# Optimization experiments

Hardware: AMD Instinct MI355X
Metric: run time of the kernel (lower is better)

The kernel has to match this reference:

```python
import jax, jax.numpy as jnp
import numpy as np

DIM = 192
HEADS = 6
WS = (4, 4, 4)
N = 64          # prod(WS)
NW = 64         # windows per sample
BATCH = 2048    # num_windows * B
CPB_HIDDEN = 512


def _make_rpb_tables():
    space = len(WS)
    coords = [np.arange(-(w - 1), w, dtype=np.float32) for w in WS]
    rpb = np.stack(np.meshgrid(*coords, indexing='ij'))  # (3, 7,7,7)
    for i in range(space):
        rpb[i] = rpb[i] / (WS[i] - 1)
    rpb = np.moveaxis(rpb, 0, -1)[None]  # (1,7,7,7,3)
    rpb = 8.0 * rpb
    rpb = np.sign(rpb) * np.log2(np.abs(rpb) + 1.0) / np.log2(8.0)
    grid = np.stack(np.meshgrid(*[np.arange(w) for w in WS], indexing='ij')).reshape(space, -1)  # (3, N)
    dists = grid[:, :, None] - grid[:, None, :]  # (3, N, N)
    for i in range(space):
        center = max(int(np.prod([2 * w - 1 for w in WS[i + 1:]])), 1)
        dists[i] = (dists[i] + WS[i] - 1) * center
    rpb_idx = dists.sum(0)  # (N, N), values in [0, 343)
    return jnp.asarray(rpb, jnp.float32), jnp.asarray(rpb_idx, jnp.int32)


def setup_inputs() -> dict:
    key = jax.random.key(0)
    ks = jax.random.split(key, 8)
    rpb, rpb_idx = _make_rpb_tables()
    s = 0.02
    return {
        'x': jax.random.normal(ks[0], (BATCH, N, DIM), jnp.float32),
        'mask': jnp.zeros((NW, N, N), jnp.float32),
        'rpb': rpb,
        'rpb_idx': rpb_idx,
        'cpb_w1': jax.random.normal(ks[1], (CPB_HIDDEN, len(WS)), jnp.float32) * s,
        'cpb_b1': jnp.zeros((CPB_HIDDEN,), jnp.float32),
        'cpb_w2': jax.random.normal(ks[2], (HEADS, CPB_HIDDEN), jnp.float32) * s,
        'qkv_w': jax.random.normal(ks[3], (3 * DIM, DIM), jnp.float32) * s,
        'qkv_b': jnp.zeros((3 * DIM,), jnp.float32),
        'proj_w': jax.random.normal(ks[4], (DIM, DIM), jnp.float32) * s,
        'proj_b': jnp.zeros((DIM,), jnp.float32),
        'logit_scale': jnp.log(10.0 * jnp.ones((HEADS, 1, 1), jnp.float32)),
    }


def reference(x, mask, rpb, rpb_idx, cpb_w1, cpb_b1, cpb_w2, qkv_w, qkv_b,
              proj_w, proj_b, logit_scale):
    B, n, C = x.shape
    H = logit_scale.shape[0]
    hd = C // H
    # qkv projection -> (3, B, H, n, hd)
    qkv = (x @ qkv_w.T + qkv_b).reshape(B, n, 3, H, hd).transpose(2, 0, 3, 1, 4)
    q, k, v = qkv[0], qkv[1], qkv[2]
    # continuous position bias MLP: (1,7,7,7,3) -> (1,7,7,7,H) -> gather -> (1,H,n,n)
    h1 = jax.nn.relu(rpb @ cpb_w1.T + cpb_b1)
    bias = (h1 @ cpb_w2.T).reshape(-1, H)            # (343, H)
    bias = bias[rpb_idx.reshape(-1)].reshape(n, n, H)
    bias = 16.0 * jax.nn.sigmoid(bias)
    bias = bias.transpose(2, 0, 1)[None]             # (1, H, n, n)
    # cosine attention
    qn = q / jnp.maximum(jnp.linalg.norm(q, axis=-1, keepdims=True), 1e-12)
    kn = k / jnp.maximum(jnp.linalg.norm(k, axis=-1, keepdims=True), 1e-12)
    scale = jnp.exp(jnp.minimum(logit_scale, jnp.log(jnp.float32(100.0))))  # clamp max=log(1/0.01)
    attn = jnp.einsum('bhnd,bhmd->bhnm', qn, kn) * scale + bias
    nW = mask.shape[0]
    attn = attn + jnp.tile(mask[:, None, :, :], (B // nW, 1, 1, 1))  # (B,1,n,n) broadcast over heads
    attn = jax.nn.softmax(attn, axis=-1)
    out = jnp.einsum('bhnm,bhmd->bhnd', attn, v)
    out = out.transpose(0, 2, 1, 3).reshape(B, n, C)  # heads-major concat (b n (h c))
    return out @ proj_w.T + proj_b
```

## Files before the change

### kernel.cpp

```cpp
#include <hip/hip_runtime.h>
#include <hip/hip_bf16.h>

#define DIM 192
#define HEADS 6
#define HD 32
#define NTOK 64
#define BATCH 2048
#define CPBH 512
#define TBL 343
#define NW 64

typedef unsigned int u32;
typedef __attribute__((ext_vector_type(8))) short b16x8;
typedef __attribute__((ext_vector_type(4))) float f32x4;

__device__ __forceinline__ unsigned short f2bf(float f) {
  union { __hip_bfloat16 h; unsigned short s; } cv;
  cv.h = __float2bfloat16(f);
  return cv.s;
}
__device__ __forceinline__ u32 pack2(float a, float b) {
  return (u32)f2bf(a) | ((u32)f2bf(b) << 16);
}
union FragU { u32 u[4]; b16x8 s; uint4 q; };

__device__ __forceinline__ b16x8 ld_frag_g(const u32* p) {
  FragU f; f.q = *(const uint4*)p; return f.s;
}

__global__ __launch_bounds__(64) void k_cpb1(
    const float* __restrict__ rpb, const float* __restrict__ w1,
    const float* __restrict__ b1, const float* __restrict__ w2,
    float* __restrict__ tab) {
  int t = blockIdx.x, lane = threadIdx.x;
  float r0 = rpb[t*3], r1 = rpb[t*3+1], r2 = rpb[t*3+2];
  float a[HEADS];
  #pragma unroll
  for (int h = 0; h < HEADS; ++h) a[h] = 0.f;
  #pragma unroll
  for (int kk = 0; kk < 8; ++kk) {
    int k = lane * 8 + kk;
    float hv = fmaf(r0, w1[k*3], fmaf(r1, w1[k*3+1], fmaf(r2, w1[k*3+2], b1[k])));
    hv = fmaxf(hv, 0.f);
    #pragma unroll
    for (int h = 0; h < HEADS; ++h) a[h] = fmaf(hv, w2[h*CPBH + k], a[h]);
  }
  #pragma unroll
  for (int h = 0; h < HEADS; ++h) {
    a[h] += __shfl_xor(a[h], 1);  a[h] += __shfl_xor(a[h], 2);
    a[h] += __shfl_xor(a[h], 4);  a[h] += __shfl_xor(a[h], 8);
    a[h] += __shfl_xor(a[h], 16); a[h] += __shfl_xor(a[h], 32);
  }
  if (lane == 0) {
    #pragma unroll
    for (int h = 0; h < HEADS; ++h) tab[t*HEADS + h] = a[h];
  }
}

__global__ void k_bm(const float* __restrict__ tab, const int* __restrict__ ridx,
                     const float* __restrict__ mask, float* __restrict__ bm) {
  int idx = blockIdx.x * blockDim.x + threadIdx.x;
  if (idx >= NW * HEADS * 4096) return;
  int ij = idx & 4095;
  int h = (idx >> 12) % HEADS;
  int nw = idx / (HEADS * 4096);
  float v = tab[ridx[ij] * HEADS + h];
  bm[idx] = 16.f / (1.f + __expf(-v)) + mask[nw * 4096 + ij];
}

__global__ void k_wcvt(const float* __restrict__ qkvw, const float* __restrict__ pw,
                       u32* __restrict__ wq, u32* __restrict__ wp) {
  int i = blockIdx.x * blockDim.x + threadIdx.x;
  if (i < 55296) {
    wq[i] = pack2(qkvw[2*i], qkvw[2*i+1]);
  } else if (i < 55296 + 18432) {
    int j = i - 55296;
    wp[j] = pack2(pw[2*j], pw[2*j+1]);
  }
}

__global__ __launch_bounds__(384) void k_qkv(
    const float* __restrict__ x, const u32* __restrict__ wq,
    const float* __restrict__ bias,
    u32* __restrict__ qo, u32* __restrict__ ko, u32* __restrict__ vT) {
  __shared__ u32 xl[NTOK * 101];
  const int tid = threadIdx.x;
  const int b = blockIdx.x;
  const float4* xg = (const float4*)(x + (size_t)b * (NTOK * DIM));
  for (int i = tid; i < (NTOK * DIM) / 4; i += 384) {
    float4 v = xg[i];
    int flat = i * 4, tok = flat / DIM, k = flat % DIM;
    xl[tok*101 + k/2]     = pack2(v.x, v.y);
    xl[tok*101 + k/2 + 1] = pack2(v.z, v.w);
  }
  __syncthreads();
  const int lane = tid & 63;
  const int wv = tid >> 6;
  const int m = lane & 15;
  const int qd = lane >> 4;
  const int sel = wv >> 1;
  u32* dst = (sel == 0) ? qo : (sel == 1) ? ko : vT;
  #pragma unroll 1
  for (int p = 0; p < 3; ++p) {
    const int h = (wv & 1) * 3 + p;
    const int jbase = wv * 96 + p * 32;
    b16x8 afr[2][6];
    float bv[2][4];
    #pragma unroll
    for (int half = 0; half < 2; ++half) {
      const u32* wp = wq + (size_t)(jbase + half*16 + m) * 96;
      #pragma unroll
      for (int ks = 0; ks < 6; ++ks) afr[half][ks] = ld_frag_g(wp + ks*16 + qd*4);
      #pragma unroll
      for (int r = 0; r < 4; ++r) bv[half][r] = bias[jbase + half*16 + qd*4 + r];
    }
    const size_t bh1024 = ((size_t)b * HEADS + h) * 1024;
    #pragma unroll 1
    for (int tp = 0; tp < 2; ++tp) {
      f32x4 acc[2][2];
      #pragma unroll
      for (int tt = 0; tt < 2; ++tt) {
        acc[tt][0] = (f32x4){0.f,0.f,0.f,0.f};
        acc[tt][1] = (f32x4){0.f,0.f,0.f,0.f};
      }
      #pragma unroll
      for (int ks = 0; ks < 6; ++ks) {
        #pragma unroll
        for (int tt = 0; tt < 2; ++tt) {
          b16x8 bfr = *(const b16x8*)(&xl[((tp*2+tt)*16 + m)*101 + ks*16 + qd*4]);
          acc[tt][0] = __builtin_amdgcn_mfma_f32_16x16x32_bf16(afr[0][ks], bfr, acc[tt][0], 0,0,0);
          acc[tt][1] = __builtin_amdgcn_mfma_f32_16x16x32_bf16(afr[1][ks], bfr, acc[tt][1], 0,0,0);
        }
      }
      #pragma unroll
      for (int tt = 0; tt < 2; ++tt) {
        const int t = tp*2 + tt;
        f32x4 acc0 = acc[tt][0], acc1 = acc[tt][1];
        #pragma unroll
        for (int r = 0; r < 4; ++r) { acc0[r] += bv[0][r]; acc1[r] += bv[1][r]; }
        if (sel < 2) {
          float ss = 0.f;
          #pragma unroll
          for (int r = 0; r < 4; ++r) ss = fmaf(acc0[r],acc0[r], fmaf(acc1[r],acc1[r], ss));
          ss += __shfl_xor(ss, 16);
          ss += __shfl_xor(ss, 32);
          float inv = 1.f / fmaxf(sqrtf(ss), 1e-12f);
          #pragma unroll
          for (int r = 0; r < 4; ++r) { acc0[r] *= inv; acc1[r] *= inv; }
          int tok = t*16 + m;
          u32* o = dst + bh1024 + tok*16;
          *(uint2*)(o + qd*2)     = make_uint2(pack2(acc0[0],acc0[1]), pack2(acc0[2],acc0[3]));
          *(uint2*)(o + 8 + qd*2) = make_uint2(pack2(acc1[0],acc1[1]), pack2(acc1[2],acc1[3]));
        } else {
          float p0[8];
          #pragma unroll
          for (int r = 0; r < 4; ++r) { p0[r] = acc0[r]; p0[4+r] = acc1[r]; }
          float pr[8];
          #pragma unroll
          for (int e = 0; e < 8; ++e) pr[e] = __shfl_xor(p0[e], 1);
          if ((m & 1) == 0) {
            #pragma unroll
            for (int e = 0; e < 8; ++e) {
              int d = (e >> 2)*16 + qd*4 + (e & 3);
              dst[bh1024 + d*32 + (t*16 + m)/2] = pack2(p0[e], pr[e]);
            }
          }
        }
      }
    }
  }
}

__global__ __launch_bounds__(384) void k_attn_proj(
    const u32* __restrict__ qo, const u32* __restrict__ ko, const u32* __restrict__ vT,
    const float* __restrict__ bm, const float* __restrict__ ls,
    const u32* __restrict__ wp, const float* __restrict__ pb,
    float* __restrict__ out) {
  __shared__ u32 pbuf[HEADS][64 * 35];
  __shared__ u32 aol[64 * 99];
  const int tid = threadIdx.x;
  const int b = blockIdx.x;
  const int h = tid >> 6;
  const int lane = tid & 63;
  const int m = lane & 15, qd = lane >> 4;
  const size_t bh1024 = ((size_t)b * HEADS + h) * 1024;

  b16x8 qfr[4], kfr[4];
  #pragma unroll
  for (int mt = 0; mt < 4; ++mt) qfr[mt] = ld_frag_g(qo + bh1024 + (mt*16 + m)*16 + qd*4);
  #pragma unroll
  for (int ct = 0; ct < 4; ++ct) kfr[ct] = ld_frag_g(ko + bh1024 + (ct*16 + m)*16 + qd*4);

  f32x4 s[4][4];
  #pragma unroll
  for (int mt = 0; mt < 4; ++mt)
    #pragma unroll
    for (int ct = 0; ct < 4; ++ct) {
      f32x4 z = {0.f,0.f,0.f,0.f};
      s[mt][ct] = __builtin_amdgcn_mfma_f32_16x16x32_bf16(qfr[mt], kfr[ct], z, 0,0,0);
    }

  const float sc = __expf(fminf(ls[h], 4.60517019f));
  const float* bmp = bm + ((size_t)(b & 63) * HEADS + h) * 4096;
  #pragma unroll
  for (int mt = 0; mt < 4; ++mt)
    #pragma unroll
    for (int ct = 0; ct < 4; ++ct) {
      #pragma unroll
      for (int r = 0; r < 4; ++r) {
        int row = mt*16 + qd*4 + r, col = ct*16 + m;
        s[mt][ct][r] = fmaf(s[mt][ct][r], sc, bmp[row*64 + col]);
      }
    }
  float rinv[4][4];
  u32* pbw = pbuf[h];
  #pragma unroll
  for (int mt = 0; mt < 4; ++mt) {
    #pragma unroll
    for (int r = 0; r < 4; ++r) {
      float mm = s[mt][0][r];
      #pragma unroll
      for (int ct = 1; ct < 4; ++ct) mm = fmaxf(mm, s[mt][ct][r]);
      mm = fmaxf(mm, __shfl_xor(mm, 1)); mm = fmaxf(mm, __shfl_xor(mm, 2));
      mm = fmaxf(mm, __shfl_xor(mm, 4)); mm = fmaxf(mm, __shfl_xor(mm, 8));
      float l = 0.f;
      #pragma unroll
      for (int ct = 0; ct < 4; ++ct) { s[mt][ct][r] = __expf(s[mt][ct][r] - mm); l += s[mt][ct][r]; }
      l += __shfl_xor(l, 1); l += __shfl_xor(l, 2);
      l += __shfl_xor(l, 4); l += __shfl_xor(l, 8);
      rinv[mt][r] = 1.f / l;
      int row = mt*16 + qd*4 + r;
      #pragma unroll
      for (int ct = 0; ct < 4; ++ct) {
        float pv = s[mt][ct][r];
        float pn = __shfl_xor(pv, 1);
        if ((m & 1) == 0) pbw[row*35 + ct*8 + (m >> 1)] = pack2(pv, pn);
      }
    }
  }
  b16x8 vfr[2][2];
  #pragma unroll
  for (int nt = 0; nt < 2; ++nt)
    #pragma unroll
    for (int ks = 0; ks < 2; ++ks)
      vfr[nt][ks] = ld_frag_g(vT + bh1024 + (nt*16 + m)*32 + ks*16 + qd*4);
  #pragma unroll
  for (int mt = 0; mt < 4; ++mt) {
    b16x8 pa0 = *(const b16x8*)(&pbw[(mt*16 + m)*35 + qd*4]);
    b16x8 pa1 = *(const b16x8*)(&pbw[(mt*16 + m)*35 + 16 + qd*4]);
    #pragma unroll
    for (int nt = 0; nt < 2; ++nt) {
      f32x4 o = {0.f,0.f,0.f,0.f};
      o = __builtin_amdgcn_mfma_f32_16x16x32_bf16(pa0, vfr[nt][0], o, 0,0,0);
      o = __builtin_amdgcn_mfma_f32_16x16x32_bf16(pa1, vfr[nt][1], o, 0,0,0);
      #pragma unroll
      for (int r = 0; r < 4; ++r) {
        float val = o[r] * rinv[mt][r];
        float pn = __shfl_xor(val, 1);
        if ((m & 1) == 0) {
          int row = mt*16 + qd*4 + r;
          aol[row*99 + h*16 + nt*8 + (m >> 1)] = pack2(val, pn);
        }
      }
    }
  }
  __syncthreads();
  const int wv = h;
  b16x8 afr[2][6];
  float bv[2][4];
  #pragma unroll
  for (int jj = 0; jj < 2; ++jj) {
    const u32* wrow = wp + (size_t)((wv*2 + jj)*16 + m) * 96;
    #pragma unroll
    for (int ks = 0; ks < 6; ++ks) afr[jj][ks] = ld_frag_g(wrow + ks*16 + qd*4);
    #pragma unroll
    for (int r = 0; r < 4; ++r) bv[jj][r] = pb[(wv*2 + jj)*16 + qd*4 + r];
  }
  #pragma unroll 1
  for (int t = 0; t < 4; ++t) {
    f32x4 acc0 = {0.f,0.f,0.f,0.f}, acc1 = {0.f,0.f,0.f,0.f};
    #pragma unroll
    for (int ks = 0; ks < 6; ++ks) {
      b16x8 bfr = *(const b16x8*)(&aol[(t*16 + m)*99 + ks*16 + qd*4]);
      acc0 = __builtin_amdgcn_mfma_f32_16x16x32_bf16(afr[0][ks], bfr, acc0, 0,0,0);
      acc1 = __builtin_amdgcn_mfma_f32_16x16x32_bf16(afr[1][ks], bfr, acc1, 0,0,0);
    }
    float* op = out + ((size_t)b*64 + t*16 + m) * DIM;
    *(float4*)(op + (wv*2+0)*16 + qd*4) =
        make_float4(acc0[0]+bv[0][0], acc0[1]+bv[0][1], acc0[2]+bv[0][2], acc0[3]+bv[0][3]);
    *(float4*)(op + (wv*2+1)*16 + qd*4) =
        make_float4(acc1[0]+bv[1][0], acc1[1]+bv[1][1], acc1[2]+bv[1][2], acc1[3]+bv[1][3]);
  }
}

extern "C" void kernel_launch(void* const* d_in, const int* in_sizes, int n_in,
                              void* d_out, int out_size, void* d_ws, size_t ws_size,
                              hipStream_t stream) {
  const float* x    = (const float*)d_in[0];
  const float* mask = (const float*)d_in[1];
  const float* rpb  = (const float*)d_in[2];
  const int*   ridx = (const int*)d_in[3];
  const float* w1   = (const float*)d_in[4];
  const float* b1   = (const float*)d_in[5];
  const float* w2   = (const float*)d_in[6];
  const float* qkvw = (const float*)d_in[7];
  const float* qkvb = (const float*)d_in[8];
  const float* pw   = (const float*)d_in[9];
  const float* pb   = (const float*)d_in[10];
  const float* ls   = (const float*)d_in[11];
  float* out = (float*)d_out;

  char* ws = (char*)d_ws;
  const size_t QS = (size_t)BATCH * HEADS * NTOK * HD * 2;
  u32* qo = (u32*)(ws);
  u32* ko = (u32*)(ws + QS);
  u32* vT = (u32*)(ws + 2 * QS);
  float* btab = (float*)(ws + 3 * QS);
  float* bm   = (float*)(ws + 3 * QS + 16384);
  u32* wq = (u32*)(ws + 3 * QS + 16384 + 6291456);
  u32* wp = (u32*)(ws + 3 * QS + 16384 + 6291456 + 221184);

  k_cpb1<<<TBL, 64, 0, stream>>>(rpb, w1, b1, w2, btab);
  k_wcvt<<<(73728 + 255) / 256, 256, 0, stream>>>(qkvw, pw, wq, wp);
  k_bm<<<(NW * HEADS * 4096 + 255) / 256, 256, 0, stream>>>(btab, ridx, mask, bm);
  k_qkv<<<BATCH, 384, 0, stream>>>(x, wq, qkvb, qo, ko, vT);
  k_attn_proj<<<BATCH, 384, 0, stream>>>(qo, ko, vT, bm, ls, wp, pb, out);
}
```

Baseline: 418.2 us.

## Fuse QKV projection and attention+proj into one kernel keeping Q/K/V in LDS

```diff
diff --git a/kernel.cpp b/kernel.cpp
--- a/kernel.cpp
+++ b/kernel.cpp
@@ -27,6 +27,9 @@
 __device__ __forceinline__ b16x8 ld_frag_g(const u32* p) {
   FragU f; f.q = *(const uint4*)p; return f.s;
 }
+__device__ __forceinline__ b16x8 ld_frag_b32(const u32* p) {
+  FragU f; f.u[0] = p[0]; f.u[1] = p[1]; f.u[2] = p[2]; f.u[3] = p[3]; return f.s;
+}
 
 __global__ __launch_bounds__(64) void k_cpb1(
     const float* __restrict__ rpb, const float* __restrict__ w1,
@@ -57,15 +60,17 @@
   }
 }
 
-__global__ void k_bm(const float* __restrict__ tab, const int* __restrict__ ridx,
-                     const float* __restrict__ mask, float* __restrict__ bm) {
+__global__ void k_bmt(const float* __restrict__ tab, const int* __restrict__ ridx,
+                      const float* __restrict__ mask, float* __restrict__ bmt) {
   int idx = blockIdx.x * blockDim.x + threadIdx.x;
   if (idx >= NW * HEADS * 4096) return;
-  int ij = idx & 4095;
+  int cr = idx & 4095;
+  int col = cr >> 6, row = cr & 63;
   int h = (idx >> 12) % HEADS;
   int nw = idx / (HEADS * 4096);
+  int ij = row * 64 + col;
   float v = tab[ridx[ij] * HEADS + h];
-  bm[idx] = 16.f / (1.f + __expf(-v)) + mask[nw * 4096 + ij];
+  bmt[idx] = 16.f / (1.f + __expf(-v)) + mask[nw * 4096 + ij];
 }
 
 __global__ void k_wcvt(const float* __restrict__ qkvw, const float* __restrict__ pw,
@@ -79,82 +84,86 @@
   }
 }
 
-__global__ __launch_bounds__(384) void k_qkv(
+__global__ __launch_bounds__(384, 3) void k_mega(
     const float* __restrict__ x, const u32* __restrict__ wq,
-    const float* __restrict__ bias,
-    u32* __restrict__ qo, u32* __restrict__ ko, u32* __restrict__ vT) {
-  __shared__ u32 xl[NTOK * 101];
+    const float* __restrict__ qkvb, const float* __restrict__ bmt,
+    const float* __restrict__ ls, const u32* __restrict__ wp,
+    const float* __restrict__ pb, float* __restrict__ out) {
+  __shared__ alignas(16) u32 regA[13056];
+  __shared__ alignas(16) u32 regB[6912];
   const int tid = threadIdx.x;
   const int b = blockIdx.x;
-  const float4* xg = (const float4*)(x + (size_t)b * (NTOK * DIM));
-  for (int i = tid; i < (NTOK * DIM) / 4; i += 384) {
-    float4 v = xg[i];
-    int flat = i * 4, tok = flat / DIM, k = flat % DIM;
-    xl[tok*101 + k/2]     = pack2(v.x, v.y);
-    xl[tok*101 + k/2 + 1] = pack2(v.z, v.w);
-  }
-  __syncthreads();
+  const int h = tid >> 6;
   const int lane = tid & 63;
-  const int wv = tid >> 6;
-  const int m = lane & 15;
-  const int qd = lane >> 4;
-  const int sel = wv >> 1;
-  u32* dst = (sel == 0) ? qo : (sel == 1) ? ko : vT;
+  const int m = lane & 15, qd = lane >> 4;
+  u32* qh = regA + h * 2176;
+  u32* kh = qh + 1088;
+  u32* Ph = qh;
+  u32* vh = regB + h * 1152;
+  u32* aol = regA;
+
+  const float* xw = x + (size_t)b * (NTOK * DIM);
   #pragma unroll 1
-  for (int p = 0; p < 3; ++p) {
-    const int h = (wv & 1) * 3 + p;
-    const int jbase = wv * 96 + p * 32;
-    b16x8 afr[2][6];
-    float bv[2][4];
-    #pragma unroll
-    for (int half = 0; half < 2; ++half) {
-      const u32* wp = wq + (size_t)(jbase + half*16 + m) * 96;
-      #pragma unroll
-      for (int ks = 0; ks < 6; ++ks) afr[half][ks] = ld_frag_g(wp + ks*16 + qd*4);
-      #pragma unroll
-      for (int r = 0; r < 4; ++r) bv[half][r] = bias[jbase + half*16 + qd*4 + r];
-    }
-    const size_t bh1024 = ((size_t)b * HEADS + h) * 1024;
+  for (int tp = 0; tp < 2; ++tp) {
+    b16x8 xf[2][6];
+    #pragma unroll
+    for (int tt = 0; tt < 2; ++tt) {
+      const float* xr = xw + ((tp*2 + tt)*16 + m) * DIM + qd * 8;
+      #pragma unroll
+      for (int ks = 0; ks < 6; ++ks) {
+        float4 f0 = *(const float4*)(xr + ks*32);
+        float4 f1 = *(const float4*)(xr + ks*32 + 4);
+        FragU fu;
+        fu.u[0] = pack2(f0.x, f0.y); fu.u[1] = pack2(f0.z, f0.w);
+        fu.u[2] = pack2(f1.x, f1.y); fu.u[3] = pack2(f1.z, f1.w);
+        xf[tt][ks] = fu.s;
+      }
+    }
     #pragma unroll 1
-    for (int tp = 0; tp < 2; ++tp) {
+    for (int sel = 0; sel < 3; ++sel) {
       f32x4 acc[2][2];
-      #pragma unroll
-      for (int tt = 0; tt < 2; ++tt) {
-        acc[tt][0] = (f32x4){0.f,0.f,0.f,0.f};
-        acc[tt][1] = (f32x4){0.f,0.f,0.f,0.f};
-      }
-      #pragma unroll
-      for (int ks = 0; ks < 6; ++ks) {
+      float bv[2][4];
+      #pragma unroll
+      for (int half = 0; half < 2; ++half) {
+        b16x8 af[6];
+        const u32* wrow = wq + (size_t)(sel*192 + h*32 + half*16 + m) * 96;
         #pragma unroll
-        for (int tt = 0; tt < 2; ++tt) {
-          b16x8 bfr = *(const b16x8*)(&xl[((tp*2+tt)*16 + m)*101 + ks*16 + qd*4]);
-          acc[tt][0] = __builtin_amdgcn_mfma_f32_16x16x32_bf16(afr[0][ks], bfr, acc[tt][0], 0,0,0);
-          acc[tt][1] = __builtin_amdgcn_mfma_f32_16x16x32_bf16(afr[1][ks], bfr, acc[tt][1], 0,0,0);
+        for (int ks = 0; ks < 6; ++ks) af[ks] = ld_frag_g(wrow + ks*16 + qd*4);
+        #pragma unroll
+        for (int r = 0; r < 4; ++r) bv[half][r] = qkvb[sel*192 + h*32 + half*16 + qd*4 + r];
+        acc[half][0] = (f32x4){0.f,0.f,0.f,0.f};
+        acc[half][1] = (f32x4){0.f,0.f,0.f,0.f};
+        #pragma unroll
+        for (int ks = 0; ks < 6; ++ks) {
+          acc[half][0] = __builtin_amdgcn_mfma_f32_16x16x32_bf16(af[ks], xf[0][ks], acc[half][0], 0,0,0);
+          acc[half][1] = __builtin_amdgcn_mfma_f32_16x16x32_bf16(af[ks], xf[1][ks], acc[half][1], 0,0,0);
         }
       }
       #pragma unroll
       for (int tt = 0; tt < 2; ++tt) {
         const int t = tp*2 + tt;
-        f32x4 acc0 = acc[tt][0], acc1 = acc[tt][1];
+        f32x4 a0 = acc[0][tt], a1 = acc[1][tt];
         #pragma unroll
-        for (int r = 0; r < 4; ++r) { acc0[r] += bv[0][r]; acc1[r] += bv[1][r]; }
+        for (int r = 0; r < 4; ++r) { a0[r] += bv[0][r]; a1[r] += bv[1][r]; }
         if (sel < 2) {
           float ss = 0.f;
           #pragma unroll
-          for (int r = 0; r < 4; ++r) ss = fmaf(acc0[r],acc0[r], fmaf(acc1[r],acc1[r], ss));
+          for (int r = 0; r < 4; ++r) ss = fmaf(a0[r], a0[r], fmaf(a1[r], a1[r], ss));
           ss += __shfl_xor(ss, 16);
           ss += __shfl_xor(ss, 32);
           float inv = 1.f / fmaxf(sqrtf(ss), 1e-12f);
           #pragma unroll
-          for (int r = 0; r < 4; ++r) { acc0[r] *= inv; acc1[r] *= inv; }
-          int tok = t*16 + m;
-          u32* o = dst + bh1024 + tok*16;
-          *(uint2*)(o + qd*2)     = make_uint2(pack2(acc0[0],acc0[1]), pack2(acc0[2],acc0[3]));
-          *(uint2*)(o + 8 + qd*2) = make_uint2(pack2(acc1[0],acc1[1]), pack2(acc1[2],acc1[3]));
+          for (int r = 0; r < 4; ++r) { a0[r] *= inv; a1[r] *= inv; }
+          u32* dst = (sel == 0) ? qh : kh;
+          u32* o = dst + (t*16 + m) * 17;
+          o[qd*2]     = pack2(a0[0], a0[1]);
+          o[qd*2 + 1] = pack2(a0[2], a0[3]);
+          o[8 + qd*2]     = pack2(a1[0], a1[1]);
+          o[8 + qd*2 + 1] = pack2(a1[2], a1[3]);
         } else {
           float p0[8];
           #pragma unroll
-          for (int r = 0; r < 4; ++r) { p0[r] = acc0[r]; p0[4+r] = acc1[r]; }
+          for (int r = 0; r < 4; ++r) { p0[r] = a0[r]; p0[4+r] = a1[r]; }
           float pr[8];
           #pragma unroll
           for (int e = 0; e < 8; ++e) pr[e] = __shfl_xor(p0[e], 1);
@@ -162,34 +171,19 @@
             #pragma unroll
             for (int e = 0; e < 8; ++e) {
               int d = (e >> 2)*16 + qd*4 + (e & 3);
-              dst[bh1024 + d*32 + (t*16 + m)/2] = pack2(p0[e], pr[e]);
+              vh[d*36 + t*8 + (m >> 1)] = pack2(p0[e], pr[e]);
             }
           }
         }
       }
     }
   }
-}
-
-__global__ __launch_bounds__(384) void k_attn_proj(
-    const u32* __restrict__ qo, const u32* __restrict__ ko, const u32* __restrict__ vT,
-    const float* __restrict__ bm, const float* __restrict__ ls,
-    const u32* __restrict__ wp, const float* __restrict__ pb,
-    float* __restrict__ out) {
-  __shared__ u32 pbuf[HEADS][64 * 35];
-  __shared__ u32 aol[64 * 99];
-  const int tid = threadIdx.x;
-  const int b = blockIdx.x;
-  const int h = tid >> 6;
-  const int lane = tid & 63;
-  const int m = lane & 15, qd = lane >> 4;
-  const size_t bh1024 = ((size_t)b * HEADS + h) * 1024;
 
   b16x8 qfr[4], kfr[4];
   #pragma unroll
-  for (int mt = 0; mt < 4; ++mt) qfr[mt] = ld_frag_g(qo + bh1024 + (mt*16 + m)*16 + qd*4);
-  #pragma unroll
-  for (int ct = 0; ct < 4; ++ct) kfr[ct] = ld_frag_g(ko + bh1024 + (ct*16 + m)*16 + qd*4);
+  for (int mt = 0; mt < 4; ++mt) qfr[mt] = ld_frag_b32(qh + (mt*16 + m)*17 + qd*4);
+  #pragma unroll
+  for (int ct = 0; ct < 4; ++ct) kfr[ct] = ld_frag_b32(kh + (ct*16 + m)*17 + qd*4);
 
   f32x4 s[4][4];
   #pragma unroll
@@ -201,19 +195,19 @@
     }
 
   const float sc = __expf(fminf(ls[h], 4.60517019f));
-  const float* bmp = bm + ((size_t)(b & 63) * HEADS + h) * 4096;
+  const float* bmp = bmt + ((size_t)(b & 63) * HEADS + h) * 4096;
   #pragma unroll
   for (int mt = 0; mt < 4; ++mt)
     #pragma unroll
     for (int ct = 0; ct < 4; ++ct) {
-      #pragma unroll
-      for (int r = 0; r < 4; ++r) {
-        int row = mt*16 + qd*4 + r, col = ct*16 + m;
-        s[mt][ct][r] = fmaf(s[mt][ct][r], sc, bmp[row*64 + col]);
-      }
-    }
+      float4 bb = *(const float4*)(bmp + (ct*16 + m)*64 + mt*16 + qd*4);
+      s[mt][ct][0] = fmaf(s[mt][ct][0], sc, bb.x);
+      s[mt][ct][1] = fmaf(s[mt][ct][1], sc, bb.y);
+      s[mt][ct][2] = fmaf(s[mt][ct][2], sc, bb.z);
+      s[mt][ct][3] = fmaf(s[mt][ct][3], sc, bb.w);
+    }
+
   float rinv[4][4];
-  u32* pbw = pbuf[h];
   #pragma unroll
   for (int mt = 0; mt < 4; ++mt) {
     #pragma unroll
@@ -234,62 +228,74 @@
       for (int ct = 0; ct < 4; ++ct) {
         float pv = s[mt][ct][r];
         float pn = __shfl_xor(pv, 1);
-        if ((m & 1) == 0) pbw[row*35 + ct*8 + (m >> 1)] = pack2(pv, pn);
-      }
-    }
-  }
+        if ((m & 1) == 0) Ph[row*33 + ct*8 + (m >> 1)] = pack2(pv, pn);
+      }
+    }
+  }
+
   b16x8 vfr[2][2];
   #pragma unroll
   for (int nt = 0; nt < 2; ++nt)
     #pragma unroll
     for (int ks = 0; ks < 2; ++ks)
-      vfr[nt][ks] = ld_frag_g(vT + bh1024 + (nt*16 + m)*32 + ks*16 + qd*4);
+      vfr[nt][ks] = ld_frag_g(vh + (nt*16 + m)*36 + ks*16 + qd*4);
+  f32x4 o[4][2];
   #pragma unroll
   for (int mt = 0; mt < 4; ++mt) {
-    b16x8 pa0 = *(const b16x8*)(&pbw[(mt*16 + m)*35 + qd*4]);
-    b16x8 pa1 = *(const b16x8*)(&pbw[(mt*16 + m)*35 + 16 + qd*4]);
+    b16x8 pa0 = ld_frag_b32(Ph + (mt*16 + m)*33 + qd*4);
+    b16x8 pa1 = ld_frag_b32(Ph + (mt*16 + m)*33 + 16 + qd*4);
     #pragma unroll
     for (int nt = 0; nt < 2; ++nt) {
-      f32x4 o = {0.f,0.f,0.f,0.f};
-      o = __builtin_amdgcn_mfma_f32_16x16x32_bf16(pa0, vfr[nt][0], o, 0,0,0);
-      o = __builtin_amdgcn_mfma_f32_16x16x32_bf16(pa1, vfr[nt][1], o, 0,0,0);
+      f32x4 acc = {0.f,0.f,0.f,0.f};
+      acc = __builtin_amdgcn_mfma_f32_16x16x32_bf16(pa0, vfr[nt][0], acc, 0,0,0);
+      acc = __builtin_amdgcn_mfma_f32_16x16x32_bf16(pa1, vfr[nt][1], acc, 0,0,0);
+      o[mt][nt] = acc;
+    }
+  }
+
+  __syncthreads();
+
+  #pragma unroll
+  for (int mt = 0; mt < 4; ++mt)
+    #pragma unroll
+    for (int nt = 0; nt < 2; ++nt) {
       #pragma unroll
       for (int r = 0; r < 4; ++r) {
-        float val = o[r] * rinv[mt][r];
+        float val = o[mt][nt][r] * rinv[mt][r];
         float pn = __shfl_xor(val, 1);
         if ((m & 1) == 0) {
           int row = mt*16 + qd*4 + r;
-          aol[row*99 + h*16 + nt*8 + (m >> 1)] = pack2(val, pn);
+          aol[row*100 + h*16 + nt*8 + (m >> 1)] = pack2(val, pn);
         }
       }
     }
-  }
+
   __syncthreads();
-  const int wv = h;
-  b16x8 afr[2][6];
-  float bv[2][4];
+
+  b16x8 afp[2][6];
+  float bvp[2][4];
   #pragma unroll
   for (int jj = 0; jj < 2; ++jj) {
-    const u32* wrow = wp + (size_t)((wv*2 + jj)*16 + m) * 96;
-    #pragma unroll
-    for (int ks = 0; ks < 6; ++ks) afr[jj][ks] = ld_frag_g(wrow + ks*16 + qd*4);
-    #pragma unroll
-    for (int r = 0; r < 4; ++r) bv[jj][r] = pb[(wv*2 + jj)*16 + qd*4 + r];
+    const u32* wrow = wp + (size_t)((h*2 + jj)*16 + m) * 96;
+    #pragma unroll
+    for (int ks = 0; ks < 6; ++ks) afp[jj][ks] = ld_frag_g(wrow + ks*16 + qd*4);
+    #pragma unroll
+    for (int r = 0; r < 4; ++r) bvp[jj][r] = pb[(h*2 + jj)*16 + qd*4 + r];
   }
   #pragma unroll 1
   for (int t = 0; t < 4; ++t) {
     f32x4 acc0 = {0.f,0.f,0.f,0.f}, acc1 = {0.f,0.f,0.f,0.f};
     #pragma unroll
     for (int ks = 0; ks < 6; ++ks) {
-      b16x8 bfr = *(const b16x8*)(&aol[(t*16 + m)*99 + ks*16 + qd*4]);
-      acc0 = __builtin_amdgcn_mfma_f32_16x16x32_bf16(afr[0][ks], bfr, acc0, 0,0,0);
-      acc1 = __builtin_amdgcn_mfma_f32_16x16x32_bf16(afr[1][ks], bfr, acc1, 0,0,0);
+      b16x8 bfr = ld_frag_g(aol + (t*16 + m)*100 + ks*16 + qd*4);
+      acc0 = __builtin_amdgcn_mfma_f32_16x16x32_bf16(afp[0][ks], bfr, acc0, 0,0,0);
+      acc1 = __builtin_amdgcn_mfma_f32_16x16x32_bf16(afp[1][ks], bfr, acc1, 0,0,0);
     }
     float* op = out + ((size_t)b*64 + t*16 + m) * DIM;
-    *(float4*)(op + (wv*2+0)*16 + qd*4) =
-        make_float4(acc0[0]+bv[0][0], acc0[1]+bv[0][1], acc0[2]+bv[0][2], acc0[3]+bv[0][3]);
-    *(float4*)(op + (wv*2+1)*16 + qd*4) =
-        make_float4(acc1[0]+bv[1][0], acc1[1]+bv[1][1], acc1[2]+bv[1][2], acc1[3]+bv[1][3]);
+    *(float4*)(op + (h*2+0)*16 + qd*4) =
+        make_float4(acc0[0]+bvp[0][0], acc0[1]+bvp[0][1], acc0[2]+bvp[0][2], acc0[3]+bvp[0][3]);
+    *(float4*)(op + (h*2+1)*16 + qd*4) =
+        make_float4(acc1[0]+bvp[1][0], acc1[1]+bvp[1][1], acc1[2]+bvp[1][2], acc1[3]+bvp[1][3]);
   }
 }
 
@@ -311,18 +317,13 @@
   float* out = (float*)d_out;
 
   char* ws = (char*)d_ws;
-  const size_t QS = (size_t)BATCH * HEADS * NTOK * HD * 2;
-  u32* qo = (u32*)(ws);
-  u32* ko = (u32*)(ws + QS);
-  u32* vT = (u32*)(ws + 2 * QS);
-  float* btab = (float*)(ws + 3 * QS);
-  float* bm   = (float*)(ws + 3 * QS + 16384);
-  u32* wq = (u32*)(ws + 3 * QS + 16384 + 6291456);
-  u32* wp = (u32*)(ws + 3 * QS + 16384 + 6291456 + 221184);
+  float* btab = (float*)(ws);
+  float* bmt  = (float*)(ws + 16384);
+  u32* wq = (u32*)(ws + 16384 + 6291456);
+  u32* wp = (u32*)(ws + 16384 + 6291456 + 221184);
 
   k_cpb1<<<TBL, 64, 0, stream>>>(rpb, w1, b1, w2, btab);
   k_wcvt<<<(73728 + 255) / 256, 256, 0, stream>>>(qkvw, pw, wq, wp);
-  k_bm<<<(NW * HEADS * 4096 + 255) / 256, 256, 0, stream>>>(btab, ridx, mask, bm);
-  k_qkv<<<BATCH, 384, 0, stream>>>(x, wq, qkvb, qo, ko, vT);
-  k_attn_proj<<<BATCH, 384, 0, stream>>>(qo, ko, vT, bm, ls, wp, pb, out);
-}
+  k_bmt<<<(NW * HEADS * 4096 + 255) / 256, 256, 0, stream>>>(btab, ridx, mask, bmt);
+  k_mega<<<BATCH, 384, 0, stream>>>(x, wq, qkvb, bmt, ls, wp, pb, out);
+}
```

Result: slower. 488.8 us (+16.9%).
